# Performance work log

Measured on AMD Instinct MI355X. Metric: run time of the kernel, lower is better.

## Reference

```python
import jax, jax.numpy as jnp
import numpy as np

B, T, C, H = 8, 1024, 1024, 16
D = C // H  # head dim = 64

def setup_inputs() -> dict:
    key = jax.random.key(0)
    k1, k2, k3 = jax.random.split(key, 3)
    x = jax.random.normal(k1, (B, T, C), dtype=jnp.float32)
    W_attn = jax.random.normal(k2, (C, 3 * C), dtype=jnp.float32) * (1.0 / np.sqrt(C))
    W_proj = jax.random.normal(k3, (C, C), dtype=jnp.float32) * (1.0 / np.sqrt(C))
    # Llama RoPE frequencies: base^(-2i/D)
    omega = (10000.0 ** (-jnp.arange(0, D, 2, dtype=jnp.float32) / D))  # [D/2]
    return {"x": x, "W_attn": W_attn, "W_proj": W_proj, "omega": omega}

def _apply_rope(x, omega):
    # x: [B, T, H, D]; omega: [D/2]
    t = x.shape[1]
    ang = jnp.arange(t, dtype=x.dtype)[:, None] * omega[None, :]  # [T, D/2]
    cos = jnp.cos(ang)[None, :, None, :]  # [1, T, 1, D/2]
    sin = jnp.sin(ang)[None, :, None, :]
    d2 = x.shape[-1] // 2
    x1, x2 = x[..., :d2], x[..., d2:]
    return jnp.concatenate([x1 * cos - x2 * sin, x2 * cos + x1 * sin], axis=-1)

def reference(x, W_attn, W_proj, omega):
    b, t, c = x.shape
    qkv = jnp.einsum('btc,cd->btd', x, W_attn)  # fused QKV projection
    q, k, v = jnp.split(qkv, 3, axis=-1)
    q = q.reshape(b, t, H, D)
    k = k.reshape(b, t, H, D)
    v = v.reshape(b, t, H, D)
    q = _apply_rope(q, omega)
    k = _apply_rope(k, omega)
    # non-causal SDPA
    scale = 1.0 / jnp.sqrt(jnp.asarray(D, dtype=x.dtype))
    scores = jnp.einsum('bqhd,bkhd->bhqk', q, k) * scale
    probs = jax.nn.softmax(scores, axis=-1)
    y = jnp.einsum('bhqk,bkhd->bqhd', probs, v).reshape(b, t, c)
    return jnp.einsum('btc,cd->btd', y, W_proj)
```

## Files before the change

kernel.cpp:

```cpp
#include <hip/hip_runtime.h>
#include <hip/hip_bf16.h>
#include <stdint.h>


typedef __attribute__((ext_vector_type(8))) short short8;
typedef __attribute__((ext_vector_type(4))) float floatx4;
typedef __attribute__((ext_vector_type(2))) unsigned int uint2v;

#define DEV static __device__ __forceinline__

#if __has_builtin(__builtin_amdgcn_exp2f)
#define EXP2(x) __builtin_amdgcn_exp2f(x)
#else
#define EXP2(x) exp2f(x)
#endif

DEV uint16_t f2bf(float f) {
  union { float f; uint32_t i; } v; v.f = f;
  uint32_t u = v.i;
  return (uint16_t)((u + 0x7fffu + ((u >> 16) & 1u)) >> 16);
}

DEV uint32_t pkbf(float a, float b) {
  __hip_bfloat162 h = __float22bfloat162_rn(make_float2(a, b));
  union { __hip_bfloat162 h; uint32_t u; } v; v.h = h;
  return v.u;
}

DEV void async_load16(const uint16_t* g, uint16_t* l) {
  __builtin_amdgcn_global_load_lds(
      (const __attribute__((address_space(1))) void*)g,
      (__attribute__((address_space(3))) void*)l, 16, 0, 0);
}

__global__ __launch_bounds__(256) void prep(
    const float* __restrict__ x, const float* __restrict__ W_attn,
    const float* __restrict__ W_proj, const float* __restrict__ omega,
    uint16_t* __restrict__ xb, uint16_t* __restrict__ Wt_attn,
    uint16_t* __restrict__ Wt_proj, float2* __restrict__ tab) {
  __shared__ uint16_t tile[64][65];
  const int blk = blockIdx.x, tid = threadIdx.x;
  if (blk < 4096) {
    const size_t base = ((size_t)blk * 256 + tid) * 8;
    floatx4 a = *(const floatx4*)(x + base);
    floatx4 b = *(const floatx4*)(x + base + 4);
    short8 s;
    s[0] = (short)f2bf(a[0]); s[1] = (short)f2bf(a[1]);
    s[2] = (short)f2bf(a[2]); s[3] = (short)f2bf(a[3]);
    s[4] = (short)f2bf(b[0]); s[5] = (short)f2bf(b[1]);
    s[6] = (short)f2bf(b[2]); s[7] = (short)f2bf(b[3]);
    *(short8*)(xb + base) = s;
  } else if (blk < 5120) {
    const float* in;
    uint16_t* out;
    int R = 1024, Ccols, bx, by;
    if (blk < 4864) {
      const int idx = blk - 4096;
      in = W_attn; out = Wt_attn; Ccols = 3072;
      bx = idx % 48; by = idx / 48;
    } else {
      const int idx = blk - 4864;
      in = W_proj; out = Wt_proj; Ccols = 1024;
      bx = idx % 16; by = idx / 16;
    }
    const int tx = tid & 63, ty = tid >> 6;
    const int c0 = bx * 64, r0 = by * 64;
    #pragma unroll
    for (int i = 0; i < 64; i += 4)
      tile[ty + i][tx] = f2bf(in[(size_t)(r0 + ty + i) * Ccols + c0 + tx]);
    __syncthreads();
    #pragma unroll
    for (int i = 0; i < 64; i += 4)
      out[(size_t)(c0 + ty + i) * R + r0 + tx] = tile[tx][ty + i];
  } else {
    const int idx = (blk - 5120) * 256 + tid;
    const int t = idx >> 5, d = idx & 31;
    float s, c;
    sincosf((float)t * omega[d], &s, &c);
    tab[idx] = make_float2(c, s);
  }
}

__global__ __launch_bounds__(512) void gemm_qkv(
    const uint16_t* __restrict__ A, const uint16_t* __restrict__ Bt,
    const float2* __restrict__ tab,
    uint16_t* __restrict__ Qr, uint16_t* __restrict__ Kr, uint16_t* __restrict__ Vt) {
  __shared__ __align__(16) uint16_t As[3 * 256 * 32];
  __shared__ __align__(16) uint16_t Bs[3 * 256 * 32];
  const int tid = threadIdx.x;
  const int wave = tid >> 6, lane = tid & 63;
  const int l15 = lane & 15, quad = lane >> 4;
  const int wrow = wave >> 2, wcol = wave & 3;
  const int sw2 = (l15 >> 1) & 3;
  const int K = 1024;

  const int bid = blockIdx.x;
  const int xcd = bid & 7, slot = bid >> 3;
  const int row0 = (xcd * 4 + (slot & 3)) * 256;
  const int col0 = (slot >> 2) * 256;

  size_t aoff[2], boff[2];
  #pragma unroll
  for (int i = 0; i < 2; i++) {
    const int e = i * 512 + tid;
    const int r = e >> 2, c = e & 3;
    const int j = c ^ ((r >> 1) & 3);
    aoff[i] = (size_t)(row0 + r) * K + j * 8;
    boff[i] = (size_t)(col0 + r) * K + j * 8;
  }
  #pragma unroll
  for (int t = 0; t < 2; t++)
    #pragma unroll
    for (int i = 0; i < 2; i++) {
      async_load16(A + aoff[i] + (size_t)t * 32, As + t * 8192 + (i * 512 + tid) * 8);
      async_load16(Bt + boff[i] + (size_t)t * 32, Bs + t * 8192 + (i * 512 + tid) * 8);
    }

  floatx4 acc[8][4];
  const floatx4 z4 = {0.f, 0.f, 0.f, 0.f};
  #pragma unroll
  for (int mi = 0; mi < 8; mi++)
    #pragma unroll
    for (int ni = 0; ni < 4; ni++) acc[mi][ni] = z4;

  asm volatile("s_waitcnt vmcnt(4)" ::: "memory");
  __builtin_amdgcn_s_barrier();

  int qa = 0, q2 = 2;
  const int arow = wrow * 128 + l15;
  const int brow = wcol * 64 + l15;
  for (int kt = 0; kt < 32; ++kt) {
    const uint16_t* Aq = As + qa * 8192;
    const uint16_t* Bq = Bs + qa * 8192;
    uint16_t* As2 = As + q2 * 8192;
    uint16_t* Bs2 = Bs + q2 * 8192;

    short8 af[8], bfr[4];
    #pragma unroll
    for (int mi = 0; mi < 8; mi++)
      af[mi] = *(const short8*)(Aq + (arow + mi * 16) * 32 + ((quad ^ sw2) * 8));
    #pragma unroll
    for (int ni = 0; ni < 4; ni++)
      bfr[ni] = *(const short8*)(Bq + (brow + ni * 16) * 32 + ((quad ^ sw2) * 8));
    if (kt < 30) {
      const size_t k2 = (size_t)(kt + 2) * 32;
      #pragma unroll
      for (int i = 0; i < 2; i++) {
        async_load16(A + aoff[i] + k2, As2 + (i * 512 + tid) * 8);
        async_load16(Bt + boff[i] + k2, Bs2 + (i * 512 + tid) * 8);
      }
    }
    __builtin_amdgcn_s_barrier();
    asm volatile("s_waitcnt lgkmcnt(0)" ::: "memory");
    __builtin_amdgcn_s_setprio(1);
    #pragma unroll
    for (int mi = 0; mi < 8; mi++)
      #pragma unroll
      for (int ni = 0; ni < 4; ni++)
        acc[mi][ni] = __builtin_amdgcn_mfma_f32_16x16x32_bf16(
            af[mi], bfr[ni], acc[mi][ni], 0, 0, 0);
    __builtin_amdgcn_s_setprio(0);
    if (kt < 30) {
      asm volatile("s_waitcnt vmcnt(4)" ::: "memory");
    } else if (kt == 30) {
      asm volatile("s_waitcnt vmcnt(0)" ::: "memory");
    }
    __builtin_amdgcn_s_barrier();
    qa = (qa == 2) ? 0 : qa + 1;
    q2 = (q2 == 2) ? 0 : q2 + 1;
  }

  const int cblk = col0 + wcol * 64;
  const int region = cblk >> 10;
  const int h = (cblk & 1023) >> 6;
  const int rr = row0 + wrow * 128;
  const int b = rr >> 10;
  const int tbase = rr & 1023;
  const size_t bh = (size_t)b * 16 + h;

  if (region < 2) {
    uint16_t* dst = (region == 0) ? Qr : Kr;
    const float scl = (region == 0) ? 0.125f * 1.44269504088896f : 1.0f;
    #pragma unroll
    for (int mi = 0; mi < 8; mi++)
      #pragma unroll
      for (int r = 0; r < 4; r++) {
        const int t = tbase + mi * 16 + quad * 4 + r;
        const size_t base = (bh * 1024 + t) * 64;
        const float2 cs0 = tab[t * 32 + l15];
        const float2 cs1 = tab[t * 32 + l15 + 16];
        {
          float x1 = acc[mi][0][r], x2 = acc[mi][2][r];
          dst[base + l15]      = f2bf((x1 * cs0.x - x2 * cs0.y) * scl);
          dst[base + l15 + 32] = f2bf((x2 * cs0.x + x1 * cs0.y) * scl);
        }
        {
          float x1 = acc[mi][1][r], x2 = acc[mi][3][r];
          dst[base + 16 + l15]      = f2bf((x1 * cs1.x - x2 * cs1.y) * scl);
          dst[base + 16 + l15 + 32] = f2bf((x2 * cs1.x + x1 * cs1.y) * scl);
        }
      }
  } else {
    #pragma unroll
    for (int mi = 0; mi < 8; mi++)
      #pragma unroll
      for (int ni = 0; ni < 4; ni++) {
        const int d = ni * 16 + l15;
        #pragma unroll
        for (int r = 0; r < 4; r++) {
          const int t = tbase + mi * 16 + quad * 4 + r;
          Vt[bh * 65536 + (size_t)d * 1024 + t] = f2bf(acc[mi][ni][r]);
        }
      }
  }
}

DEV void gemm_core8(const uint16_t* __restrict__ Ag,
                    const uint16_t* __restrict__ Bg,
                    int row0, int col0,
                    uint16_t* As, uint16_t* Bs, floatx4 (&acc)[4][4]) {
  const int tid = threadIdx.x;
  const int wave = tid >> 6, lane = tid & 63;
  const int l15 = lane & 15, quad = lane >> 4;
  const int wrow = wave >> 1, wcol = wave & 1;
  const int sw = l15 & 7;
  const int K = 1024;

  size_t aoff[4], boff[2];
  #pragma unroll
  for (int i = 0; i < 4; i++) {
    const int e = i * 512 + tid;
    const int r = e >> 3, c = e & 7, j = c ^ (r & 7);
    aoff[i] = (size_t)(row0 + r) * K + j * 8;
  }
  #pragma unroll
  for (int i = 0; i < 2; i++) {
    const int e = i * 512 + tid;
    const int r = e >> 3, c = e & 7, j = c ^ (r & 7);
    boff[i] = (size_t)(col0 + r) * K + j * 8;
  }

  #pragma unroll
  for (int t = 0; t < 2; t++) {
    #pragma unroll
    for (int i = 0; i < 2; i++)
      async_load16(Bg + boff[i] + (size_t)t * 64, Bs + t * 8192 + (i * 512 + tid) * 8);
    #pragma unroll
    for (int i = 0; i < 4; i++)
      async_load16(Ag + aoff[i] + (size_t)t * 64, As + t * 16384 + (i * 512 + tid) * 8);
  }

  const floatx4 z4 = {0.f, 0.f, 0.f, 0.f};
  #pragma unroll
  for (int mi = 0; mi < 4; mi++)
    #pragma unroll
    for (int ni = 0; ni < 4; ni++) acc[mi][ni] = z4;

  asm volatile("s_waitcnt vmcnt(6)" ::: "memory");
  __builtin_amdgcn_s_barrier();

  int qa = 0, q2 = 2;
  const int arow = wrow * 64 + l15;
  const int brow = wcol * 64 + l15;
  for (int kt = 0; kt < 16; ++kt) {
    const uint16_t* Aq = As + qa * 16384;
    const uint16_t* Bq = Bs + qa * 8192;
    uint16_t* As2 = As + q2 * 16384;
    uint16_t* Bs2 = Bs + q2 * 8192;
    const size_t k2 = (size_t)(kt + 2) * 64;

    short8 af[4], bfr[4];
    #pragma unroll
    for (int mi = 0; mi < 4; mi++)
      af[mi] = *(const short8*)(Aq + (arow + mi * 16) * 64 + ((quad ^ sw) * 8));
    #pragma unroll
    for (int ni = 0; ni < 4; ni++)
      bfr[ni] = *(const short8*)(Bq + (brow + ni * 16) * 64 + ((quad ^ sw) * 8));
    if (kt < 14) {
      #pragma unroll
      for (int i = 0; i < 2; i++)
        async_load16(Bg + boff[i] + k2, Bs2 + (i * 512 + tid) * 8);
      #pragma unroll
      for (int i = 0; i < 2; i++)
        async_load16(Ag + aoff[i] + k2, As2 + (i * 512 + tid) * 8);
    }
    __builtin_amdgcn_s_barrier();
    asm volatile("s_waitcnt lgkmcnt(0)" ::: "memory");
    __builtin_amdgcn_s_setprio(1);
    #pragma unroll
    for (int mi = 0; mi < 4; mi++)
      #pragma unroll
      for (int ni = 0; ni < 4; ni++)
        acc[mi][ni] = __builtin_amdgcn_mfma_f32_16x16x32_bf16(
            af[mi], bfr[ni], acc[mi][ni], 0, 0, 0);
    __builtin_amdgcn_s_setprio(0);
    __builtin_amdgcn_s_barrier();

    #pragma unroll
    for (int mi = 0; mi < 4; mi++)
      af[mi] = *(const short8*)(Aq + (arow + mi * 16) * 64 + (((4 + quad) ^ sw) * 8));
    #pragma unroll
    for (int ni = 0; ni < 4; ni++)
      bfr[ni] = *(const short8*)(Bq + (brow + ni * 16) * 64 + (((4 + quad) ^ sw) * 8));
    if (kt < 14) {
      #pragma unroll
      for (int i = 2; i < 4; i++)
        async_load16(Ag + aoff[i] + k2, As2 + (i * 512 + tid) * 8);
      asm volatile("s_waitcnt vmcnt(6)" ::: "memory");
    } else if (kt == 14) {
      asm volatile("s_waitcnt vmcnt(0)" ::: "memory");
    }
    __builtin_amdgcn_s_barrier();
    asm volatile("s_waitcnt lgkmcnt(0)" ::: "memory");
    __builtin_amdgcn_s_setprio(1);
    #pragma unroll
    for (int mi = 0; mi < 4; mi++)
      #pragma unroll
      for (int ni = 0; ni < 4; ni++)
        acc[mi][ni] = __builtin_amdgcn_mfma_f32_16x16x32_bf16(
            af[mi], bfr[ni], acc[mi][ni], 0, 0, 0);
    __builtin_amdgcn_s_setprio(0);
    __builtin_amdgcn_s_barrier();

    qa = (qa == 2) ? 0 : qa + 1;
    q2 = (q2 == 2) ? 0 : q2 + 1;
  }
}

__global__ __launch_bounds__(512) void gemm_out(
    const uint16_t* __restrict__ A, const uint16_t* __restrict__ Bt,
    float* __restrict__ Cmat, int M, int N, int K) {
  __shared__ __align__(16) uint16_t As[3 * 256 * 64];
  __shared__ __align__(16) uint16_t Bs[3 * 128 * 64];
  const int bid = blockIdx.x;
  const int xcd = bid & 7, slot = bid >> 3;
  const int row0 = (xcd * 4 + (slot & 3)) * 256;
  const int col0 = (slot >> 2) * 128;
  floatx4 acc[4][4];
  gemm_core8(A, Bt, row0, col0, As, Bs, acc);

  const int tid = threadIdx.x;
  const int wave = tid >> 6, lane = tid & 63;
  const int l15 = lane & 15, quad = lane >> 4;
  #pragma unroll
  for (int mi = 0; mi < 4; mi++)
    #pragma unroll
    for (int ni = 0; ni < 4; ni++) {
      const int col = col0 + (wave & 1) * 64 + ni * 16 + l15;
      #pragma unroll
      for (int r = 0; r < 4; r++) {
        const int row = row0 + (wave >> 1) * 64 + mi * 16 + quad * 4 + r;
        Cmat[(size_t)row * N + col] = acc[mi][ni][r];
      }
    }
}

#define FLD 72

__global__ __launch_bounds__(256) void flash_attn(
    const uint16_t* __restrict__ Qr, const uint16_t* __restrict__ Kr,
    const uint16_t* __restrict__ Vt, uint16_t* __restrict__ Y) {
  __shared__ uint16_t Ks[64 * 64];
  __shared__ uint16_t Vs[64 * 64];
  __shared__ uint16_t Ps[128 * FLD];
  const int tid = threadIdx.x;
  const int wv = tid >> 6, lane = tid & 63;
  const int l15 = lane & 15, quad = lane >> 4;
  const int sw = l15 & 7;
  const int bh = blockIdx.x & 127, qt = blockIdx.x >> 7;
  const int b = bh >> 4, h = bh & 15;
  const int q0 = qt * 128;
  const uint16_t* Qbh = Qr + (size_t)bh * 1024 * 64;
  const uint16_t* Kbh = Kr + (size_t)bh * 1024 * 64;
  const uint16_t* Vbh = Vt + (size_t)bh * 64 * 1024;

  short8 bq[2][2];
  #pragma unroll
  for (int g = 0; g < 2; g++)
    #pragma unroll
    for (int ks = 0; ks < 2; ks++)
      bq[g][ks] = *(const short8*)(Qbh +
          (size_t)(q0 + wv * 32 + g * 16 + l15) * 64 + ks * 32 + quad * 8);

  float psum[2] = {0.f, 0.f};
  const floatx4 z4 = {0.f, 0.f, 0.f, 0.f};
  floatx4 oacc[2][4];
  #pragma unroll
  for (int g = 0; g < 2; g++)
    #pragma unroll
    for (int mi = 0; mi < 4; mi++) oacc[g][mi] = z4;

  for (int kt = 0; kt < 16; kt++) {
    __syncthreads();
    #pragma unroll
    for (int i = 0; i < 2; i++) {
      const int e = i * 256 + tid;
      const int r = e >> 3;
      const int j = (e & 7) ^ (r & 7);
      async_load16(Kbh + (size_t)(kt * 64 + r) * 64 + j * 8, Ks + e * 8);
      async_load16(Vbh + (size_t)r * 1024 + kt * 64 + j * 8, Vs + e * 8);
    }
    __syncthreads();

    #pragma unroll
    for (int g = 0; g < 2; g++) {
      const int qrow = wv * 32 + g * 16 + l15;
      floatx4 sacc[4];
      #pragma unroll
      for (int ni = 0; ni < 4; ni++) {
        sacc[ni] = z4;
        #pragma unroll
        for (int ks = 0; ks < 2; ks++) {
          short8 ak = *(const short8*)(&Ks[(ni * 16 + l15) * 64 +
                                           (((ks * 4 + quad) ^ sw) * 8)]);
          sacc[ni] = __builtin_amdgcn_mfma_f32_16x16x32_bf16(ak, bq[g][ks], sacc[ni], 0, 0, 0);
        }
      }
      #pragma unroll
      for (int ni = 0; ni < 4; ni++) {
        float p0 = EXP2(sacc[ni][0]), p1 = EXP2(sacc[ni][1]);
        float p2 = EXP2(sacc[ni][2]), p3 = EXP2(sacc[ni][3]);
        psum[g] += (p0 + p1) + (p2 + p3);
        uint2v pk; pk[0] = pkbf(p0, p1); pk[1] = pkbf(p2, p3);
        *(uint2v*)(&Ps[qrow * FLD + ni * 16 + quad * 4]) = pk;
      }
      short8 bp[2];
      #pragma unroll
      for (int ks = 0; ks < 2; ks++)
        bp[ks] = *(const short8*)(&Ps[qrow * FLD + ks * 32 + quad * 8]);
      #pragma unroll
      for (int mi = 0; mi < 4; mi++) {
        #pragma unroll
        for (int ks = 0; ks < 2; ks++) {
          short8 av = *(const short8*)(&Vs[(mi * 16 + l15) * 64 +
                                           (((ks * 4 + quad) ^ sw) * 8)]);
          oacc[g][mi] = __builtin_amdgcn_mfma_f32_16x16x32_bf16(av, bp[ks], oacc[g][mi], 0, 0, 0);
        }
      }
    }
  }

  #pragma unroll
  for (int g = 0; g < 2; g++) {
    float l_tot = psum[g];
    l_tot += __shfl_xor(l_tot, 16, 64);
    l_tot += __shfl_xor(l_tot, 32, 64);
    const float linv = 1.0f / l_tot;
    const int t = q0 + wv * 32 + g * 16 + l15;
    #pragma unroll
    for (int mi = 0; mi < 4; mi++) {
      uint2v yk;
      yk[0] = pkbf(oacc[g][mi][0] * linv, oacc[g][mi][1] * linv);
      yk[1] = pkbf(oacc[g][mi][2] * linv, oacc[g][mi][3] * linv);
      *(uint2v*)(Y + (size_t)(b * 1024 + t) * 1024 + h * 64 + mi * 16 + quad * 4) = yk;
    }
  }
}

extern "C" void kernel_launch(void* const* d_in, const int* in_sizes, int n_in,
                              void* d_out, int out_size, void* d_ws, size_t ws_size,
                              hipStream_t stream) {
  const float* x      = (const float*)d_in[0];
  const float* W_attn = (const float*)d_in[1];
  const float* W_proj = (const float*)d_in[2];
  const float* omega  = (const float*)d_in[3];
  float* out = (float*)d_out;

  uint16_t* wsp     = (uint16_t*)d_ws;
  uint16_t* xb      = wsp;
  uint16_t* Wt_attn = xb + (size_t)8192 * 1024;
  uint16_t* Wt_proj = Wt_attn + (size_t)3072 * 1024;
  uint16_t* Qr      = Wt_proj + (size_t)1024 * 1024;
  uint16_t* Kr      = Qr + (size_t)128 * 1024 * 64;
  uint16_t* Vt      = Kr + (size_t)128 * 1024 * 64;
  float2*   ropet   = (float2*)(Vt + (size_t)128 * 1024 * 64);
  uint16_t* Y       = xb;

  prep<<<5248, 256, 0, stream>>>(x, W_attn, W_proj, omega, xb, Wt_attn, Wt_proj, ropet);
  gemm_qkv<<<384, 512, 0, stream>>>(xb, Wt_attn, ropet, Qr, Kr, Vt);
  flash_attn<<<1024, 256, 0, stream>>>(Qr, Kr, Vt, Y);
  gemm_out<<<256, 512, 0, stream>>>(Y, Wt_proj, out, 8192, 1024, 1024);
}
```

Measured before the change: 243.9 us.

## Restructure QKV GEMM mainloop to double-buffered BK=64 with four-phase interleaved loads

Changes the QKV projection GEMM from a triple-buffered K-step of 32 to a double-buffered K-step of 64, with a wider 8-way XOR swizzle in shared memory. Each iteration is split into four phases that interleave LDS fragment reads, staggered global prefetch chunks (A, then B half 0, then B half 1) and MFMA bursts, each phase separated by barriers. The aim is to halve the number of loop iterations and spread global-load issue across the compute phases. In exchange it adds many more barriers per iteration and a full vmcnt(0) drain at the end of each step, which may expose memory latency.

```diff
diff --git a/kernel.cpp b/kernel.cpp
--- a/kernel.cpp
+++ b/kernel.cpp
@@ -85,13 +85,13 @@
     const uint16_t* __restrict__ A, const uint16_t* __restrict__ Bt,
     const float2* __restrict__ tab,
     uint16_t* __restrict__ Qr, uint16_t* __restrict__ Kr, uint16_t* __restrict__ Vt) {
-  __shared__ __align__(16) uint16_t As[3 * 256 * 32];
-  __shared__ __align__(16) uint16_t Bs[3 * 256 * 32];
+  __shared__ __align__(16) uint16_t As[2 * 256 * 64];
+  __shared__ __align__(16) uint16_t Bs[2 * 256 * 64];
   const int tid = threadIdx.x;
   const int wave = tid >> 6, lane = tid & 63;
   const int l15 = lane & 15, quad = lane >> 4;
   const int wrow = wave >> 2, wcol = wave & 3;
-  const int sw2 = (l15 >> 1) & 3;
+  const int sw = l15 & 7;
   const int K = 1024;
 
   const int bid = blockIdx.x;
@@ -99,22 +99,30 @@
   const int row0 = (xcd * 4 + (slot & 3)) * 256;
   const int col0 = (slot >> 2) * 256;
 
-  size_t aoff[2], boff[2];
+  size_t aoff[4], boff[2];
+  #pragma unroll
+  for (int i = 0; i < 4; i++) {
+    const int e = i * 512 + tid;
+    const int r = e >> 3, c = e & 7, j = c ^ (r & 7);
+    aoff[i] = (size_t)(row0 + r) * K + j * 8;
+  }
   #pragma unroll
   for (int i = 0; i < 2; i++) {
     const int e = i * 512 + tid;
-    const int r = e >> 2, c = e & 3;
-    const int j = c ^ ((r >> 1) & 3);
-    aoff[i] = (size_t)(row0 + r) * K + j * 8;
-    boff[i] = (size_t)(col0 + r) * K + j * 8;
-  }
-  #pragma unroll
-  for (int t = 0; t < 2; t++)
-    #pragma unroll
-    for (int i = 0; i < 2; i++) {
-      async_load16(A + aoff[i] + (size_t)t * 32, As + t * 8192 + (i * 512 + tid) * 8);
-      async_load16(Bt + boff[i] + (size_t)t * 32, Bs + t * 8192 + (i * 512 + tid) * 8);
-    }
+    const int r = e >> 3, c = e & 7, j = c ^ (r & 7);
+    boff[i] = (size_t)r * K + j * 8;
+  }
+  const size_t bbase0 = (size_t)col0 * K;
+  const size_t bbase1 = (size_t)(col0 + 128) * K;
+
+  #pragma unroll
+  for (int i = 0; i < 4; i++)
+    async_load16(A + aoff[i], As + (i * 512 + tid) * 8);
+  #pragma unroll
+  for (int i = 0; i < 2; i++) {
+    async_load16(Bt + bbase0 + boff[i], Bs + (i * 512 + tid) * 8);
+    async_load16(Bt + bbase1 + boff[i], Bs + 8192 + (i * 512 + tid) * 8);
+  }
 
   floatx4 acc[8][4];
   const floatx4 z4 = {0.f, 0.f, 0.f, 0.f};
@@ -123,51 +131,101 @@
     #pragma unroll
     for (int ni = 0; ni < 4; ni++) acc[mi][ni] = z4;
 
-  asm volatile("s_waitcnt vmcnt(4)" ::: "memory");
+  asm volatile("s_waitcnt vmcnt(0)" ::: "memory");
   __builtin_amdgcn_s_barrier();
 
-  int qa = 0, q2 = 2;
   const int arow = wrow * 128 + l15;
   const int brow = wcol * 64 + l15;
-  for (int kt = 0; kt < 32; ++kt) {
-    const uint16_t* Aq = As + qa * 8192;
-    const uint16_t* Bq = Bs + qa * 8192;
-    uint16_t* As2 = As + q2 * 8192;
-    uint16_t* Bs2 = Bs + q2 * 8192;
-
-    short8 af[8], bfr[4];
-    #pragma unroll
-    for (int mi = 0; mi < 8; mi++)
-      af[mi] = *(const short8*)(Aq + (arow + mi * 16) * 32 + ((quad ^ sw2) * 8));
+  for (int kt = 0; kt < 16; ++kt) {
+    const int set = kt & 1;
+    const uint16_t* Aq = As + set * 16384;
+    const uint16_t* Bq = Bs + set * 16384;
+    uint16_t* An = As + (set ^ 1) * 16384;
+    uint16_t* Bn = Bs + (set ^ 1) * 16384;
+    const size_t kk = (size_t)(kt + 1) * 64;
+    short8 bf0[4], af[4];
+
     #pragma unroll
     for (int ni = 0; ni < 4; ni++)
-      bfr[ni] = *(const short8*)(Bq + (brow + ni * 16) * 32 + ((quad ^ sw2) * 8));
-    if (kt < 30) {
-      const size_t k2 = (size_t)(kt + 2) * 32;
-      #pragma unroll
-      for (int i = 0; i < 2; i++) {
-        async_load16(A + aoff[i] + k2, As2 + (i * 512 + tid) * 8);
-        async_load16(Bt + boff[i] + k2, Bs2 + (i * 512 + tid) * 8);
-      }
+      bf0[ni] = *(const short8*)(Bq + (brow + ni * 16) * 64 + ((quad ^ sw) * 8));
+    #pragma unroll
+    for (int m = 0; m < 4; m++)
+      af[m] = *(const short8*)(Aq + (arow + m * 16) * 64 + ((quad ^ sw) * 8));
+    if (kt < 15) {
+      #pragma unroll
+      for (int i = 0; i < 4; i++)
+        async_load16(A + aoff[i] + kk, An + (i * 512 + tid) * 8);
     }
     __builtin_amdgcn_s_barrier();
     asm volatile("s_waitcnt lgkmcnt(0)" ::: "memory");
     __builtin_amdgcn_s_setprio(1);
     #pragma unroll
-    for (int mi = 0; mi < 8; mi++)
+    for (int m = 0; m < 4; m++)
       #pragma unroll
       for (int ni = 0; ni < 4; ni++)
-        acc[mi][ni] = __builtin_amdgcn_mfma_f32_16x16x32_bf16(
-            af[mi], bfr[ni], acc[mi][ni], 0, 0, 0);
+        acc[m][ni] = __builtin_amdgcn_mfma_f32_16x16x32_bf16(
+            af[m], bf0[ni], acc[m][ni], 0, 0, 0);
     __builtin_amdgcn_s_setprio(0);
-    if (kt < 30) {
-      asm volatile("s_waitcnt vmcnt(4)" ::: "memory");
-    } else if (kt == 30) {
-      asm volatile("s_waitcnt vmcnt(0)" ::: "memory");
-    }
-    __builtin_amdgcn_s_barrier();
-    qa = (qa == 2) ? 0 : qa + 1;
-    q2 = (q2 == 2) ? 0 : q2 + 1;
+    __builtin_amdgcn_s_barrier();
+
+    #pragma unroll
+    for (int m = 0; m < 4; m++)
+      af[m] = *(const short8*)(Aq + (arow + (m + 4) * 16) * 64 + ((quad ^ sw) * 8));
+    if (kt < 15) {
+      #pragma unroll
+      for (int i = 0; i < 2; i++)
+        async_load16(Bt + bbase0 + boff[i] + kk, Bn + (i * 512 + tid) * 8);
+    }
+    __builtin_amdgcn_s_barrier();
+    asm volatile("s_waitcnt lgkmcnt(0)" ::: "memory");
+    __builtin_amdgcn_s_setprio(1);
+    #pragma unroll
+    for (int m = 0; m < 4; m++)
+      #pragma unroll
+      for (int ni = 0; ni < 4; ni++)
+        acc[m + 4][ni] = __builtin_amdgcn_mfma_f32_16x16x32_bf16(
+            af[m], bf0[ni], acc[m + 4][ni], 0, 0, 0);
+    __builtin_amdgcn_s_setprio(0);
+    __builtin_amdgcn_s_barrier();
+
+    #pragma unroll
+    for (int ni = 0; ni < 4; ni++)
+      bf0[ni] = *(const short8*)(Bq + (brow + ni * 16) * 64 + (((4 + quad) ^ sw) * 8));
+    #pragma unroll
+    for (int m = 0; m < 4; m++)
+      af[m] = *(const short8*)(Aq + (arow + m * 16) * 64 + (((4 + quad) ^ sw) * 8));
+    if (kt < 15) {
+      #pragma unroll
+      for (int i = 0; i < 2; i++)
+        async_load16(Bt + bbase1 + boff[i] + kk, Bn + 8192 + (i * 512 + tid) * 8);
+    }
+    __builtin_amdgcn_s_barrier();
+    asm volatile("s_waitcnt lgkmcnt(0)" ::: "memory");
+    __builtin_amdgcn_s_setprio(1);
+    #pragma unroll
+    for (int m = 0; m < 4; m++)
+      #pragma unroll
+      for (int ni = 0; ni < 4; ni++)
+        acc[m][ni] = __builtin_amdgcn_mfma_f32_16x16x32_bf16(
+            af[m], bf0[ni], acc[m][ni], 0, 0, 0);
+    __builtin_amdgcn_s_setprio(0);
+    __builtin_amdgcn_s_barrier();
+
+    #pragma unroll
+    for (int m = 0; m < 4; m++)
+      af[m] = *(const short8*)(Aq + (arow + (m + 4) * 16) * 64 + (((4 + quad) ^ sw) * 8));
+    __builtin_amdgcn_s_barrier();
+    asm volatile("s_waitcnt lgkmcnt(0)" ::: "memory");
+    __builtin_amdgcn_s_setprio(1);
+    #pragma unroll
+    for (int m = 0; m < 4; m++)
+      #pragma unroll
+      for (int ni = 0; ni < 4; ni++)
+        acc[m + 4][ni] = __builtin_amdgcn_mfma_f32_16x16x32_bf16(
+            af[m], bf0[ni], acc[m + 4][ni], 0, 0, 0);
+    __builtin_amdgcn_s_setprio(0);
+    if (kt < 15) asm volatile("s_waitcnt vmcnt(0)" ::: "memory");
+    __builtin_amdgcn_s_barrier();
   }
 
   const int cblk = col0 + wcol * 64;
```

Result: no change. 248.7 us (+1.9%).
